# Kernel tuning notes

Hardware: AMD Instinct MI355X
Metric: run time of the kernel (lower is better)

The kernel has to match this reference:

```python
import jax, jax.numpy as jnp
import numpy as np

N_HEADS, N_LEVELS, N_POINTS, D_MODEL = 8, 3, 12, 64
PARAM_NAMES = ['vp0_w','vp0_b','vp1_w','vp1_b','so0_w','so0_b','so1_w','so1_b','so2_w','so2_b','so3_w','so3_b','aw0_w','aw0_b','aw1_w','aw1_b','aw2_w','aw2_b','aw3_w','aw3_b','op0_w','op0_b','op1_w','op1_b']

def _lrelu(x):
    return jnp.where(x >= 0, x, 0.1 * x)

def _conv(x, w, b):
    y = jax.lax.conv_general_dilated(x, w, (1, 1), 'SAME', dimension_numbers=('NCHW', 'OIHW', 'NCHW'))
    return y + b[None, :, None, None]

def _bilinear(img, px, py):
    # img [B,C,H,W]; px,py [B,Q] absolute pixel coords; zero padding (grid_sample 'zeros')
    B, C, H, W = img.shape
    flat = img.reshape(B, C, H * W)
    x0 = jnp.floor(px); y0 = jnp.floor(py)
    wx1 = px - x0; wy1 = py - y0
    def g(xi, yi, wgt):
        valid = (xi >= 0) & (xi <= W - 1) & (yi >= 0) & (yi <= H - 1)
        xi_c = jnp.clip(xi, 0, W - 1).astype(jnp.int32)
        yi_c = jnp.clip(yi, 0, H - 1).astype(jnp.int32)
        v = jnp.take_along_axis(flat, (yi_c * W + xi_c)[:, None, :], axis=2)
        return v * (wgt * valid)[:, None, :]
    return (g(x0, y0, (1 - wx1) * (1 - wy1)) + g(x0 + 1, y0, wx1 * (1 - wy1))
          + g(x0, y0 + 1, (1 - wx1) * wy1) + g(x0 + 1, y0 + 1, wx1 * wy1))

def _flow_warp(img, flow):
    # img [n,C,h,w]; flow [n,2,h,w] (x,y); matches grid_sample align_corners=True
    n, C, h, w = img.shape
    gy, gx = jnp.meshgrid(jnp.arange(h, dtype=img.dtype), jnp.arange(w, dtype=img.dtype), indexing='ij')
    px = (gx[None] + flow[:, 0]).reshape(n, h * w)
    py = (gy[None] + flow[:, 1]).reshape(n, h * w)
    return _bilinear(img, px, py).reshape(n, C, h, w)

def _forward(x, flow_1, flow_2, flip_flow_1, flip_flow_2, p):
    n, t, c, h, w = x.shape
    hw = h * w; THW = t * hw
    M, L, P, D = N_HEADS, N_LEVELS, N_POINTS, c // N_HEADS
    flow_cn1 = flow_1
    flow_cn2 = flow_1 + _flow_warp(flow_2, flow_1)
    flow_n1c, flow_n1n2 = flip_flow_1, flow_2
    flow_n2n1 = flip_flow_2
    flow_n2c = flip_flow_2 + _flow_warp(flip_flow_1, flip_flow_2)
    warp_cn1 = _flow_warp(x[:, 1], flow_cn1)
    warp_cn2 = _flow_warp(x[:, 2], flow_cn2)
    warp_n1c = _flow_warp(x[:, 0], flow_n1c)
    warp_n1n2 = _flow_warp(x[:, 2], flow_n1n2)
    warp_n2n1 = _flow_warp(x[:, 1], flow_n2n1)
    warp_n2c = _flow_warp(x[:, 0], flow_n2c)
    extra = jnp.concatenate([x[:, 0], warp_cn1, warp_cn2, warp_n1c, warp_n1n2, warp_n2n1, warp_n2c,
                             flow_cn1, flow_cn2, flow_n1c, flow_n1n2, flow_n2n1, flow_n2c], axis=1)
    value = _conv(_lrelu(_conv(x.reshape(n, t * c, h, w), p['vp0_w'], p['vp0_b'])), p['vp1_w'], p['vp1_b'])
    def head(e, pre):
        y = _lrelu(_conv(e, p[pre + '0_w'], p[pre + '0_b']))
        y = _lrelu(_conv(y, p[pre + '1_w'], p[pre + '1_b']))
        y = _lrelu(_conv(y, p[pre + '2_w'], p[pre + '2_b']))
        return _conv(y, p[pre + '3_w'], p[pre + '3_b'])
    so = head(extra, 'so')  # [n, L*M*L*P*2, h, w]
    aw = head(extra, 'aw')  # [n, L*M*L*P*9, h, w]
    so = so.reshape(n, t, -1, hw).transpose(0, 1, 3, 2).reshape(n, THW, M, L, P, 2)
    aw = aw.reshape(n, t, -1, hw).transpose(0, 1, 3, 2).reshape(n, THW, M, L * P * 9)
    aw = jax.nn.softmax(aw, axis=-1).reshape(n, THW, M, L, P * 9)
    # flow-guided offsets: add per-(query-frame, target-level) flow to learned offsets
    off = so.reshape(n, t, hw, M, L, P, 2)
    fz = jnp.zeros_like(flow_cn2)
    def lvl(f0, f1, f2):
        s = jnp.stack([f0, f1, f2], 1)  # [n,3,2,h,w]
        return s.transpose(0, 3, 4, 1, 2).reshape(n, hw, L, 2)[:, None, :, None, :, None, :]
    off = jnp.concatenate([
        off[:, 0:1] + lvl(fz, flow_cn1, flow_cn2),
        off[:, 1:2] + lvl(flow_n1c, fz, flow_n1n2),
        off[:, 2:3] + lvl(flow_n2c, flow_n2n1, fz)], axis=1).reshape(n, THW, M, L, P, 2)
    # 3x3 integer patch around each sampling point
    pi, pj = jnp.meshgrid(jnp.arange(-1, 2), jnp.arange(-1, 2), indexing='ij')
    patch = jnp.stack([pi, pj], -1).reshape(1, 1, 1, 1, 1, 9, 2).astype(off.dtype)
    off = (off[..., None, :] + patch).reshape(n, THW, M, L, P * 9, 2)
    # reference points (valid_ratios are all 1: full masks are zeros)
    ry, rx = jnp.meshgrid((jnp.arange(h) + 0.5) / h, (jnp.arange(w) + 0.5) / w, indexing='ij')
    ref = jnp.stack([rx, ry], -1).reshape(1, hw, 2).astype(off.dtype)
    ref = jnp.tile(ref, (1, t, 1))  # [1, THW, 2]
    norm = jnp.array([w, h], dtype=off.dtype)
    loc = ref[:, :, None, None, None, :] + off / norm  # [n,THW,M,L,P*9,2] normalized
    # multi-scale deformable attention (all L levels share (h,w)); align_corners=False, zeros pad
    P9 = P * 9
    v = value.reshape(n, t, c, hw).transpose(0, 1, 3, 2).reshape(n, THW, M, D)
    vl = v.reshape(n, L, hw, M, D).transpose(0, 3, 1, 4, 2).reshape(n * M * L, D, h, w)
    px = (loc[..., 0] * w - 0.5).transpose(0, 2, 3, 1, 4).reshape(n * M * L, THW * P9)
    py = (loc[..., 1] * h - 0.5).transpose(0, 2, 3, 1, 4).reshape(n * M * L, THW * P9)
    sampled = _bilinear(vl, px, py).reshape(n, M, L, D, THW, P9)
    out = jnp.einsum('nmldqp,nqmlp->nqmd', sampled, aw).reshape(n, THW, c)
    out = out.reshape(n, t, h, w, c).transpose(0, 1, 4, 2, 3).reshape(n, t * c, h, w)
    out = _conv(_lrelu(_conv(out, p['op0_w'], p['op0_b'])), p['op1_w'], p['op1_b'])
    return out.reshape(n, t, c, h, w) + x

def setup_inputs():
    key = jax.random.key(0)
    n, t, c, h, w = 1, 3, 64, 32, 32
    ks = jax.random.split(key, 24)
    d = {}
    d['x'] = jax.random.normal(ks[0], (n, t, c, h, w), jnp.float32)
    for i, name in enumerate(['flow_1', 'flow_2', 'flip_flow_1', 'flip_flow_2']):
        d[name] = jax.random.normal(ks[1 + i], (n, 2, h, w), jnp.float32)
    cin_extra = 7 * c + 12
    specs = [('vp0', t * c, t * c), ('vp1', t * c, t * c),
             ('so0', c, cin_extra), ('so1', c, c), ('so2', c, c), ('so3', N_LEVELS * N_HEADS * N_LEVELS * N_POINTS * 2, c),
             ('aw0', c, cin_extra), ('aw1', c, c), ('aw2', c, c), ('aw3', N_LEVELS * N_HEADS * N_LEVELS * N_POINTS * 9, c),
             ('op0', t * c, t * c), ('op1', t * c, t * c)]
    for i, (name, co, ci) in enumerate(specs):
        kw, kb = jax.random.split(ks[5 + i])
        std = (2.0 / (ci * 9)) ** 0.5
        d[name + '_w'] = jax.random.normal(kw, (co, ci, 3, 3), jnp.float32) * std
        d[name + '_b'] = jax.random.normal(kb, (co,), jnp.float32) * 0.01
    return d

def reference(x, flow_1, flow_2, flip_flow_1, flip_flow_2, vp0_w, vp0_b, vp1_w, vp1_b, so0_w, so0_b, so1_w, so1_b, so2_w, so2_b, so3_w, so3_b, aw0_w, aw0_b, aw1_w, aw1_b, aw2_w, aw2_b, aw3_w, aw3_b, op0_w, op0_b, op1_w, op1_b):
    p = dict(zip(PARAM_NAMES, (vp0_w, vp0_b, vp1_w, vp1_b, so0_w, so0_b, so1_w, so1_b, so2_w, so2_b, so3_w, so3_b, aw0_w, aw0_b, aw1_w, aw1_b, aw2_w, aw2_b, aw3_w, aw3_b, op0_w, op0_b, op1_w, op1_b)))
    return _forward(x, flow_1, flow_2, flip_flow_1, flip_flow_2, p)
```

## Files before the change

### kernel.cpp

```cpp
#include <hip/hip_runtime.h>
#include <math.h>

#define HW 1024

typedef __attribute__((ext_vector_type(8))) short bf16x8;
typedef __attribute__((ext_vector_type(4))) float floatx4;

__device__ __forceinline__ unsigned short f2bf(float f) {
    unsigned u = __float_as_uint(f);
    u += 0x7FFF + ((u >> 16) & 1);
    return (unsigned short)(u >> 16);
}
__device__ __forceinline__ float bf2f(unsigned short u) {
    return __uint_as_float(((unsigned)u) << 16);
}
__device__ __forceinline__ float bflo(unsigned u) { return __uint_as_float(u << 16); }
__device__ __forceinline__ float bfhi(unsigned u) { return __uint_as_float(u & 0xffff0000u); }

__device__ __forceinline__ float bilin32(const float* __restrict__ img, float px, float py) {
    float x0f = floorf(px), y0f = floorf(py);
    float wx = px - x0f, wy = py - y0f;
    bool vx0 = (x0f >= 0.f) && (x0f <= 31.f);
    bool vx1 = (x0f >= -1.f) && (x0f <= 30.f);
    bool vy0 = (y0f >= 0.f) && (y0f <= 31.f);
    bool vy1 = (y0f >= -1.f) && (y0f <= 30.f);
    int ix0 = (int)fminf(fmaxf(x0f, 0.f), 31.f);
    int iy0 = (int)fminf(fmaxf(y0f, 0.f), 31.f);
    int ix1 = (int)fminf(fmaxf(x0f + 1.f, 0.f), 31.f);
    int iy1 = (int)fminf(fmaxf(y0f + 1.f, 0.f), 31.f);
    float w00 = (1.f - wx) * (1.f - wy) * ((vx0 && vy0) ? 1.f : 0.f);
    float w01 = wx * (1.f - wy) * ((vx1 && vy0) ? 1.f : 0.f);
    float w10 = (1.f - wx) * wy * ((vx0 && vy1) ? 1.f : 0.f);
    float w11 = wx * wy * ((vx1 && vy1) ? 1.f : 0.f);
    return w00 * img[iy0 * 32 + ix0] + w01 * img[iy0 * 32 + ix1] +
           w10 * img[iy1 * 32 + ix0] + w11 * img[iy1 * 32 + ix1];
}

__device__ __forceinline__ float2 comp_flow(const float* __restrict__ fa,
                                            const float* __restrict__ fb, int pix) {
    int y = pix >> 5, x = pix & 31;
    float fx = fa[pix], fy = fa[HW + pix];
    float px = (float)x + fx, py = (float)y + fy;
    float2 r;
    r.x = fx + bilin32(fb, px, py);
    r.y = fy + bilin32(fb + HW, px, py);
    return r;
}

struct WD { const float* src; int cout, Cin, nCb, wbase, beg; };
struct PrepP {
    const float *x, *f1, *f2, *ff1, *ff2;
    float *fcn2, *fn2c;
    unsigned short *x_pad, *extra_pad, *wgt;
    WD wd[12];
};

__global__ __launch_bounds__(256) void prep_k(PrepP P) {
    __shared__ float wlds[16 * 288];
    const int b = blockIdx.x, tid = threadIdx.x;
    if (b < 192) {
        int idx = b * 256 + tid;
        int pix = idx / 48, c4 = idx - pix * 48;
        int y = pix >> 5, xx = pix & 31;
        int c0 = c4 * 4;
        ushort4 s;
        s.x = f2bf(P.x[(size_t)(c0 + 0) * HW + pix]);
        s.y = f2bf(P.x[(size_t)(c0 + 1) * HW + pix]);
        s.z = f2bf(P.x[(size_t)(c0 + 2) * HW + pix]);
        s.w = f2bf(P.x[(size_t)(c0 + 3) * HW + pix]);
        *(ushort4*)(&P.x_pad[(size_t)((y + 1) * 34 + xx + 1) * 192 + c0]) = s;
    } else if (b < 2112) {
        int idx = (b - 192) * 256 + tid;
        int ch = idx >> 10, pix = idx & 1023;
        int y = pix >> 5, xx = pix & 31;
        float v = 0.f;
        if (ch < 64) {
            v = P.x[(size_t)ch * HW + pix];
        } else if (ch < 448) {
            int grp = (ch - 64) >> 6;
            int c = (ch - 64) & 63;
            const float* src;
            float fx, fy;
            if (grp == 0)      { src = P.x + 64 * HW;  fx = P.f1[pix];  fy = P.f1[HW + pix]; }
            else if (grp == 1) { src = P.x + 128 * HW; float2 r = comp_flow(P.f1, P.f2, pix);  fx = r.x; fy = r.y; }
            else if (grp == 2) { src = P.x;            fx = P.ff1[pix]; fy = P.ff1[HW + pix]; }
            else if (grp == 3) { src = P.x + 128 * HW; fx = P.f2[pix];  fy = P.f2[HW + pix]; }
            else if (grp == 4) { src = P.x + 64 * HW;  fx = P.ff2[pix]; fy = P.ff2[HW + pix]; }
            else               { src = P.x;            float2 r = comp_flow(P.ff2, P.ff1, pix); fx = r.x; fy = r.y; }
            v = bilin32(src + c * HW, (float)xx + fx, (float)y + fy);
        } else if (ch < 460) {
            int fc = ch - 448;
            int which = fc >> 1, comp = fc & 1;
            if (which == 0)      v = P.f1[comp * HW + pix];
            else if (which == 1) { float2 r = comp_flow(P.f1, P.f2, pix);  v = comp ? r.y : r.x; }
            else if (which == 2) v = P.ff1[comp * HW + pix];
            else if (which == 3) v = P.f2[comp * HW + pix];
            else if (which == 4) v = P.ff2[comp * HW + pix];
            else                 { float2 r = comp_flow(P.ff2, P.ff1, pix); v = comp ? r.y : r.x; }
        }
        P.extra_pad[(size_t)((y + 1) * 34 + xx + 1) * 480 + ch] = f2bf(v);
    } else if (b < 2128) {
        int idx = (b - 2112) * 256 + tid;
        if (idx < 1024) {
            float2 r = comp_flow(P.f1, P.f2, idx);
            P.fcn2[idx] = r.x; P.fcn2[HW + idx] = r.y;
        } else if (idx < 2048) {
            int pix = idx - 1024;
            float2 r = comp_flow(P.ff2, P.ff1, pix);
            P.fn2c[pix] = r.x; P.fn2c[HW + pix] = r.y;
        }
    } else {
        int blk = b - 2128;
        int di = 0;
        while (di < 11 && blk >= P.wd[di + 1].beg) ++di;
        WD w = P.wd[di];
        int local = blk - w.beg;
        int co16 = local / w.nCb, cb = local - co16 * w.nCb;
        int cr0 = co16 * 16, ci0 = cb * 32;
        for (int i = tid; i < 16 * 288; i += 256) {
            int cr = i / 288, o = i - cr * 288;
            int crg = cr0 + cr, ci = ci0 + o / 9;
            float v = (crg < w.cout && ci < w.Cin)
                ? w.src[((size_t)crg * w.Cin + ci0) * 9 + o] : 0.f;
            wlds[i] = v;
        }
        __syncthreads();
        for (int e = tid; e < 9 * 512; e += 256) {
            int t = e >> 9, idx = e & 511;
            int j = idx & 7, lane = idx >> 3, q = lane >> 4, mm = lane & 15;
            P.wgt[((size_t)w.wbase + ((size_t)co16 * 9 + t) * w.nCb + cb) * 512 + idx] =
                f2bf(wlds[mm * 288 + (q * 8 + j) * 9 + t]);
        }
    }
}

struct CDesc {
    const unsigned short* in;
    const unsigned short* wgt;
    const float* bias;
    void* out;
    const float* residual;
    int Cpad, nCb, Cout, mode, cmod, relu, Mblocks;
};
struct CParam { CDesc d[4]; };

template<int PIXROWS>
__global__ __launch_bounds__(256) void conv_mfma_k(CParam P) {
    constexpr int TROWS = PIXROWS + 2;
    constexpr int TC = TROWS * 34 * 4;
    constexpr int ITRIPS = (TC + 255) / 256;
    constexpr int NTY = PIXROWS / 4;
    constexpr int NACC = NTY * 2;
    __shared__ unsigned short blds[TROWS * 34 * 40];
    __shared__ unsigned short wlds[36 * 512];

    int bx = blockIdx.x;
    int di = 0;
    while (bx >= P.d[di].Mblocks) { bx -= P.d[di].Mblocks; ++di; }
    const CDesc d = P.d[di];

    const int tid = threadIdx.x;
    const int w = tid >> 6, lane = tid & 63;
    const int lq = lane >> 4, ln = lane & 15;
    const int co0 = bx * 64;
    const int by = blockIdx.y, y0 = by * PIXROWS;
    const unsigned short* __restrict__ in = d.in;
    const unsigned short* __restrict__ wg = d.wgt;
    const int Cpad = d.Cpad, nCb = d.nCb;

    floatx4 acc[4][NACC];
#pragma unroll
    for (int mt = 0; mt < 4; ++mt)
#pragma unroll
        for (int nt = 0; nt < NACC; ++nt)
            acc[mt][nt] = (floatx4){0.f, 0.f, 0.f, 0.f};

    bf16x8 ireg[ITRIPS];
    bf16x8 wreg[9];

    auto load_regs = [&](int cb) {
        const int ci0 = cb << 5;
#pragma unroll
        for (int k = 0; k < ITRIPS; ++k) {
            int i = tid + k * 256;
            if (i < TC) {
                int r = i / 136, rem = i - r * 136, c = rem >> 2, g = rem & 3;
                ireg[k] = *(const bf16x8*)(in + (size_t)((y0 + r) * 34 + c) * Cpad + ci0 + g * 8);
            }
        }
#pragma unroll
        for (int k = 0; k < 9; ++k) {
            int i = tid + k * 256;
            int chunk = i >> 6, l16 = i & 63;
            int mt = chunk / 9, t = chunk - mt * 9;
            wreg[k] = *(const bf16x8*)(wg + ((size_t)(((co0 >> 4) + mt) * 9 + t) * nCb + cb) * 512 + l16 * 8);
        }
    };

    load_regs(0);

    for (int cb = 0; cb < nCb; ++cb) {
        __syncthreads();
#pragma unroll
        for (int k = 0; k < ITRIPS; ++k) {
            int i = tid + k * 256;
            if (i < TC) {
                int r = i / 136, rem = i - r * 136, c = rem >> 2, g = rem & 3;
                *(bf16x8*)(&blds[(r * 34 + c) * 40 + g * 8]) = ireg[k];
            }
        }
#pragma unroll
        for (int k = 0; k < 9; ++k) {
            int i = tid + k * 256;
            int chunk = i >> 6, l16 = i & 63;
            *(bf16x8*)(&wlds[chunk * 512 + l16 * 8]) = wreg[k];
        }
        __syncthreads();
        if (cb + 1 < nCb) load_regs(cb + 1);
        for (int t = 0; t < 9; ++t) {
            const int dy = t / 3, dx = t - dy * 3;
            bf16x8 bfr[NACC];
#pragma unroll
            for (int ty = 0; ty < NTY; ++ty)
#pragma unroll
                for (int tx = 0; tx < 2; ++tx) {
                    int yy = w * NTY + ty + dy;
                    int xx = tx * 16 + ln + dx;
                    bfr[ty * 2 + tx] = *(const bf16x8*)(&blds[(yy * 34 + xx) * 40 + lq * 8]);
                }
#pragma unroll
            for (int mt = 0; mt < 4; ++mt) {
                bf16x8 afr = *(const bf16x8*)(&wlds[(mt * 9 + t) * 512 + lane * 8]);
#pragma unroll
                for (int nt = 0; nt < NACC; ++nt)
                    acc[mt][nt] = __builtin_amdgcn_mfma_f32_16x16x32_bf16(afr, bfr[nt], acc[mt][nt], 0, 0, 0);
            }
        }
    }

#pragma unroll
    for (int mt = 0; mt < 4; ++mt) {
        const int co = co0 + mt * 16 + lq * 4;
        if (co >= d.Cout) continue;
        float bv[4];
#pragma unroll
        for (int r = 0; r < 4; ++r) bv[r] = d.bias[co + r];
#pragma unroll
        for (int nt = 0; nt < NACC; ++nt) {
            const int ty = nt >> 1, tx = nt & 1;
            const int pix = by * (PIXROWS * 32) + (w * NTY + ty) * 32 + tx * 16 + ln;
            float v[4];
#pragma unroll
            for (int r = 0; r < 4; ++r) {
                float vv = acc[mt][nt][r] + bv[r];
                if (d.relu) vv = (vv >= 0.f) ? vv : 0.1f * vv;
                v[r] = vv;
            }
            if (d.mode == 0) {
                float* o = (float*)d.out;
#pragma unroll
                for (int r = 0; r < 4; ++r) {
                    float vv = v[r];
                    if (d.residual) vv += d.residual[(size_t)(co + r) * HW + pix];
                    o[(size_t)(co + r) * HW + pix] = vv;
                }
            } else if (d.mode == 1) {
                int fq = co / d.cmod, cc = co - fq * d.cmod;
                *(float4*)((float*)d.out + ((size_t)fq * HW + pix) * d.cmod + cc) =
                    make_float4(v[0], v[1], v[2], v[3]);
            } else if (d.mode == 2) {
                int fq = co / d.cmod, cc = co - fq * d.cmod;
                ushort4 s4;
                s4.x = f2bf(v[0]); s4.y = f2bf(v[1]); s4.z = f2bf(v[2]); s4.w = f2bf(v[3]);
                *(ushort4*)((unsigned short*)d.out + ((size_t)fq * HW + pix) * d.cmod + cc) = s4;
            } else {
                int yy = (pix >> 5) + 1, xx = (pix & 31) + 1;
                ushort4 s4;
                s4.x = f2bf(v[0]); s4.y = f2bf(v[1]); s4.z = f2bf(v[2]); s4.w = f2bf(v[3]);
                *(ushort4*)((unsigned short*)d.out + (size_t)(yy * 34 + xx) * d.cmod + co) = s4;
            }
        }
    }
}

__global__ __launch_bounds__(256) void deform_attn_k(
    const unsigned short* __restrict__ value_b, const float* __restrict__ so_t,
    const unsigned short* __restrict__ aw_t,
    const float* __restrict__ flow_1, const float* __restrict__ flow_2,
    const float* __restrict__ flip_flow_1, const float* __restrict__ flip_flow_2,
    const float* __restrict__ flow_cn2, const float* __restrict__ flow_n2c,
    unsigned short* __restrict__ attn_pad)
{
    __shared__ unsigned short vlds[24576];
    __shared__ unsigned short pwlds[4][432];
    const int tid = threadIdx.x;
    const int wav = tid >> 6, lane = tid & 63;
    const int m = blockIdx.x & 7, qc = blockIdx.x >> 3;

    for (int i = tid; i < 3072; i += 256) {
        int l = i >> 10, p = i & 1023;
        *(bf16x8*)(&vlds[(size_t)i * 8]) =
            *(const bf16x8*)(value_b + ((size_t)((l * 8 + m) * 1024) + p) * 8);
    }
    __syncthreads();

    const int pp = lane & 15, gq = lane >> 4;
    const int gdy = (gq >> 1) * 2 - 1;
    const int gdx = (gq & 1) * 2 - 1;
    const bool selx = (gq & 1);
    const bool sely = (gq >> 1);

    for (int r = 0; r < 8; ++r) {
        const int q = qc * 32 + r * 4 + wav;
        const int f = q >> 10, pix = q & 1023;
        const int y = pix >> 5, x = pix & 31;

        float flx0 = 0.f, fly0 = 0.f, flx1 = 0.f, fly1 = 0.f, flx2 = 0.f, fly2 = 0.f;
        if (f == 0) {
            flx1 = flow_1[pix];      fly1 = flow_1[HW + pix];
            flx2 = flow_cn2[pix];    fly2 = flow_cn2[HW + pix];
        } else if (f == 1) {
            flx0 = flip_flow_1[pix]; fly0 = flip_flow_1[HW + pix];
            flx2 = flow_2[pix];      fly2 = flow_2[HW + pix];
        } else {
            flx0 = flow_n2c[pix];    fly0 = flow_n2c[HW + pix];
            flx1 = flip_flow_2[pix]; fly1 = flip_flow_2[HW + pix];
        }

        const unsigned short* awp = aw_t + (size_t)q * 2592 + m * 324;
        float av[6];
        float vmax = -1e30f;
#pragma unroll
        for (int it = 0; it < 6; ++it) {
            int j = lane + it * 64;
            float a = (j < 324) ? bf2f(awp[j]) : -1e30f;
            av[it] = a;
            vmax = fmaxf(vmax, a);
        }
#pragma unroll
        for (int off = 32; off; off >>= 1) vmax = fmaxf(vmax, __shfl_xor(vmax, off));
        float ssum = 0.f;
#pragma unroll
        for (int it = 0; it < 6; ++it) {
            int j = lane + it * 64;
            float e = (j < 324) ? __expf(av[it] - vmax) : 0.f;
            av[it] = e;
            ssum += e;
        }
#pragma unroll
        for (int off = 32; off; off >>= 1) ssum += __shfl_xor(ssum, off);
        const float inv = 1.f / ssum;

#pragma unroll
        for (int it = 0; it < 6; ++it) {
            int j = lane + it * 64;
            if (j < 324) {
                int pi = j / 9, k = j - pi * 9;
                pwlds[wav][pi * 12 + k] = f2bf(av[it] * inv);
            }
        }

        float acc[8];
#pragma unroll
        for (int dd = 0; dd < 8; ++dd) acc[dd] = 0.f;
        const float* sop = so_t + (size_t)q * 576 + m * 72;

#pragma unroll
        for (int pt = 0; pt < 3; ++pt) {
            int pi = pt * 16 + pp;
            if (pi < 36) {
                int l = pi / 12;
                float2 so2 = *(const float2*)(sop + pi * 2);
                float fx = (l == 0) ? flx0 : (l == 1) ? flx1 : flx2;
                float fy = (l == 0) ? fly0 : (l == 1) ? fly1 : fly2;
                float bxf = (float)x + so2.x + fx;
                float byf = (float)y + so2.y + fy;
                float x0f = floorf(bxf), y0f = floorf(byf);
                float wx = bxf - x0f, wy = byf - y0f;
                float ax = 1.f - wx, ay = 1.f - wy;
                int x0 = (int)fminf(fmaxf(x0f, -2.f), 34.f);
                int y0 = (int)fminf(fmaxf(y0f, -2.f), 34.f);

                const unsigned short* pr = &pwlds[wav][pi * 12];
                uint2 pv0 = *(const uint2*)(pr);
                uint2 pv1 = *(const uint2*)(pr + 4);
                float a0 = bflo(pv0.x), a1 = bfhi(pv0.x), a2 = bflo(pv0.y);
                float a3 = bfhi(pv0.y), a4 = bflo(pv1.x), a5 = bfhi(pv1.x);
                float a6 = bflo(pv1.y), a7 = bfhi(pv1.y), a8 = bf2f(pr[8]);

                float bs0a, bs0b, bs1a, bs1b, bs2a, bs2b;
                {
                    float b0, b1, b2, b3;
                    b0 = a0 * ax; b1 = a0 * wx + a3 * ax; b2 = a3 * wx + a6 * ax; b3 = a6 * wx;
                    bs0a = selx ? b2 : b0; bs0b = selx ? b3 : b1;
                    b0 = a1 * ax; b1 = a1 * wx + a4 * ax; b2 = a4 * wx + a7 * ax; b3 = a7 * wx;
                    bs1a = selx ? b2 : b0; bs1b = selx ? b3 : b1;
                    b0 = a2 * ax; b1 = a2 * wx + a5 * ax; b2 = a5 * wx + a8 * ax; b3 = a8 * wx;
                    bs2a = selx ? b2 : b0; bs2b = selx ? b3 : b1;
                }
                float c00, c01, c10, c11;
                {
                    float c0 = bs0a * ay, c1 = bs0a * wy + bs1a * ay;
                    float c2 = bs1a * wy + bs2a * ay, c3 = bs2a * wy;
                    c00 = sely ? c2 : c0; c10 = sely ? c3 : c1;
                    c0 = bs0b * ay; c1 = bs0b * wy + bs1b * ay;
                    c2 = bs1b * wy + bs2b * ay; c3 = bs2b * wy;
                    c01 = sely ? c2 : c0; c11 = sely ? c3 : c1;
                }
                float cg[2][2] = {{c00, c01}, {c10, c11}};
                const int vbase = l * 1024;
#pragma unroll
                for (int sy = 0; sy < 2; ++sy) {
#pragma unroll
                    for (int sx = 0; sx < 2; ++sx) {
                        int dy = gdy + sy, dx = gdx + sx;
                        float pyf = y0f + (float)dy, pxf = x0f + (float)dx;
                        bool v = (pxf >= 0.f) && (pxf <= 31.f) && (pyf >= 0.f) && (pyf <= 31.f);
                        int px = min(max(x0 + dx, 0), 31);
                        int py = min(max(y0 + dy, 0), 31);
                        float c = cg[sy][sx] * (v ? 1.f : 0.f);
                        uint4 vv = *(const uint4*)(&vlds[(size_t)(vbase + py * 32 + px) * 8]);
                        acc[0] = fmaf(c, bflo(vv.x), acc[0]);
                        acc[1] = fmaf(c, bfhi(vv.x), acc[1]);
                        acc[2] = fmaf(c, bflo(vv.y), acc[2]);
                        acc[3] = fmaf(c, bfhi(vv.y), acc[3]);
                        acc[4] = fmaf(c, bflo(vv.z), acc[4]);
                        acc[5] = fmaf(c, bfhi(vv.z), acc[5]);
                        acc[6] = fmaf(c, bflo(vv.w), acc[6]);
                        acc[7] = fmaf(c, bfhi(vv.w), acc[7]);
                    }
                }
            }
        }

#pragma unroll
        for (int dd = 0; dd < 8; ++dd) {
#pragma unroll
            for (int off = 32; off; off >>= 1) acc[dd] += __shfl_xor(acc[dd], off);
        }
        if (lane == 0) {
            unsigned short* op = attn_pad + (size_t)((y + 1) * 34 + x + 1) * 192 + f * 64 + m * 8;
            ushort4 s0, s1;
            s0.x = f2bf(acc[0]); s0.y = f2bf(acc[1]); s0.z = f2bf(acc[2]); s0.w = f2bf(acc[3]);
            s1.x = f2bf(acc[4]); s1.y = f2bf(acc[5]); s1.z = f2bf(acc[6]); s1.w = f2bf(acc[7]);
            *(ushort4*)(op) = s0;
            *(ushort4*)(op + 4) = s1;
        }
    }
}

extern "C" void kernel_launch(void* const* d_in, const int* in_sizes, int n_in,
                              void* d_out, int out_size, void* d_ws, size_t ws_size,
                              hipStream_t stream) {
    const float* x      = (const float*)d_in[0];
    const float* flow_1 = (const float*)d_in[1];
    const float* flow_2 = (const float*)d_in[2];
    const float* flip_1 = (const float*)d_in[3];
    const float* flip_2 = (const float*)d_in[4];
    const float* vp0_w = (const float*)d_in[5];  const float* vp0_b = (const float*)d_in[6];
    const float* vp1_w = (const float*)d_in[7];  const float* vp1_b = (const float*)d_in[8];
    const float* so0_w = (const float*)d_in[9];  const float* so0_b = (const float*)d_in[10];
    const float* so1_w = (const float*)d_in[11]; const float* so1_b = (const float*)d_in[12];
    const float* so2_w = (const float*)d_in[13]; const float* so2_b = (const float*)d_in[14];
    const float* so3_w = (const float*)d_in[15]; const float* so3_b = (const float*)d_in[16];
    const float* aw0_w = (const float*)d_in[17]; const float* aw0_b = (const float*)d_in[18];
    const float* aw1_w = (const float*)d_in[19]; const float* aw1_b = (const float*)d_in[20];
    const float* aw2_w = (const float*)d_in[21]; const float* aw2_b = (const float*)d_in[22];
    const float* aw3_w = (const float*)d_in[23]; const float* aw3_b = (const float*)d_in[24];
    const float* op0_w = (const float*)d_in[25]; const float* op0_b = (const float*)d_in[26];
    const float* op1_w = (const float*)d_in[27]; const float* op1_b = (const float*)d_in[28];
    float* out = (float*)d_out;
    (void)ws_size; (void)in_sizes; (void)n_in; (void)out_size;

    float* fws = (float*)d_ws;
    float* flow_cn2 = fws;
    float* flow_n2c = flow_cn2 + 2048;
    unsigned short* value_b = (unsigned short*)(flow_n2c + 2048);
    float* so_t     = (float*)(value_b + 196608);
    unsigned short* uws = (unsigned short*)(so_t + 1769472);
    unsigned short* x_pad     = uws;
    unsigned short* vp0h      = x_pad + 1156 * 192;
    unsigned short* extra_pad = vp0h + 1156 * 192;
    unsigned short* s1 = extra_pad + 1156 * 480;
    unsigned short* a1 = s1 + 1156 * 64;
    unsigned short* s2 = a1 + 1156 * 64;
    unsigned short* a2 = s2 + 1156 * 64;
    unsigned short* attn_pad = a2 + 1156 * 64;
    unsigned short* op0h     = attn_pad + 1156 * 192;
    const size_t pad_shorts = (size_t)1156 * (192 * 4 + 480 + 64 * 4);
    unsigned short* aw_t = op0h + 1156 * 192;
    unsigned short* wgt  = aw_t + (size_t)3072 * 2592;

    hipMemsetAsync(x_pad, 0, pad_shorts * sizeof(unsigned short), stream);

    PrepP pp;
    pp.x = x; pp.f1 = flow_1; pp.f2 = flow_2; pp.ff1 = flip_1; pp.ff2 = flip_2;
    pp.fcn2 = flow_cn2; pp.fn2c = flow_n2c;
    pp.x_pad = x_pad; pp.extra_pad = extra_pad; pp.wgt = wgt;
    pp.wd[0]  = {vp0_w, 192, 192, 6,     0,    0};
    pp.wd[1]  = {vp1_w, 192, 192, 6,   648,   72};
    pp.wd[2]  = {so0_w,  64, 460, 15, 1296,  144};
    pp.wd[3]  = {aw0_w,  64, 460, 15, 1836,  204};
    pp.wd[4]  = {so1_w,  64,  64, 2,  2376,  264};
    pp.wd[5]  = {aw1_w,  64,  64, 2,  2448,  272};
    pp.wd[6]  = {so2_w,  64,  64, 2,  2520,  280};
    pp.wd[7]  = {aw2_w,  64,  64, 2,  2592,  288};
    pp.wd[8]  = {so3_w, 1728, 64, 2,  2664,  296};
    pp.wd[9]  = {aw3_w, 7776, 64, 2,  4608,  512};
    pp.wd[10] = {op0_w, 192, 192, 6, 13392, 1488};
    pp.wd[11] = {op1_w, 192, 192, 6, 14040, 1560};
    prep_k<<<3760, 256, 0, stream>>>(pp);

    const int BIG = 1 << 30;
    CDesc nul = {nullptr, nullptr, nullptr, nullptr, nullptr, 0, 0, 0, 0, 0, 0, BIG};

    {
        CParam cp;
        cp.d[0] = {x_pad,     wgt + (size_t)0 * 512,    vp0_b, vp0h, nullptr, 192, 6,  192, 3, 192, 1, 3};
        cp.d[1] = {extra_pad, wgt + (size_t)1296 * 512, so0_b, s1,   nullptr, 480, 15, 64,  3, 64,  1, 1};
        cp.d[2] = {extra_pad, wgt + (size_t)1836 * 512, aw0_b, a1,   nullptr, 480, 15, 64,  3, 64,  1, 1};
        cp.d[3] = nul;
        conv_mfma_k<4><<<dim3(5, 8), 256, 0, stream>>>(cp);
    }
    {
        CParam cp;
        cp.d[0] = {vp0h, wgt + (size_t)648 * 512,  vp1_b, value_b, nullptr, 192, 6, 192, 2, 8,  0, 3};
        cp.d[1] = {s1,   wgt + (size_t)2376 * 512, so1_b, s2,      nullptr, 64,  2, 64,  3, 64, 1, 1};
        cp.d[2] = {a1,   wgt + (size_t)2448 * 512, aw1_b, a2,      nullptr, 64,  2, 64,  3, 64, 1, 1};
        cp.d[3] = nul;
        conv_mfma_k<4><<<dim3(5, 8), 256, 0, stream>>>(cp);
    }
    {
        CParam cp;
        cp.d[0] = {s2, wgt + (size_t)2520 * 512, so2_b, s1, nullptr, 64, 2, 64, 3, 64, 1, 1};
        cp.d[1] = {a2, wgt + (size_t)2592 * 512, aw2_b, a1, nullptr, 64, 2, 64, 3, 64, 1, 1};
        cp.d[2] = nul; cp.d[3] = nul;
        conv_mfma_k<4><<<dim3(2, 8), 256, 0, stream>>>(cp);
    }
    {
        CParam cp;
        cp.d[0] = {s1, wgt + (size_t)2664 * 512, so3_b, so_t, nullptr, 64, 2, 1728, 1, 576,  0, 27};
        cp.d[1] = {a1, wgt + (size_t)4608 * 512, aw3_b, aw_t, nullptr, 64, 2, 7776, 2, 2592, 0, 122};
        cp.d[2] = nul; cp.d[3] = nul;
        conv_mfma_k<8><<<dim3(149, 4), 256, 0, stream>>>(cp);
    }

    deform_attn_k<<<768, 256, 0, stream>>>(value_b, so_t, aw_t,
                                           flow_1, flow_2, flip_1, flip_2,
                                           flow_cn2, flow_n2c, attn_pad);

    {
        CParam cp;
        cp.d[0] = {attn_pad, wgt + (size_t)13392 * 512, op0_b, op0h, nullptr, 192, 6, 192, 3, 192, 1, 3};
        cp.d[1] = nul; cp.d[2] = nul; cp.d[3] = nul;
        conv_mfma_k<4><<<dim3(3, 8), 256, 0, stream>>>(cp);
    }
    {
        CParam cp;
        cp.d[0] = {op0h, wgt + (size_t)14040 * 512, op1_b, out, x, 192, 6, 192, 0, 0, 0, 3};
        cp.d[1] = nul; cp.d[2] = nul; cp.d[3] = nul;
        conv_mfma_k<4><<<dim3(3, 8), 256, 0, stream>>>(cp);
    }
}
```

Before: 291.9 us.

## Narrow conv output-channel tile to raise block count and zero only pad borders

The conv kernel gains a COBLK template parameter. The small convs now use 16 output channels per block instead of 64, so they launch four times as many blocks, which raises occupancy on a mostly idle GPU. The full-buffer hipMemsetAsync of the padded activation buffers is replaced by 16 extra prep blocks that zero only the 1-pixel halo border of each buffer. In exchange, input tiles are reloaded more often per output channel and weight reuse per block drops.

Result: faster. 269.9 us (-7.5%).

```diff
diff --git a/kernel.cpp b/kernel.cpp
--- a/kernel.cpp
+++ b/kernel.cpp
@@ -109,8 +109,23 @@
             float2 r = comp_flow(P.ff2, P.ff1, pix);
             P.fn2c[pix] = r.x; P.fn2c[HW + pix] = r.y;
         }
+    } else if (b < 2144) {
+        const int chans[9] = {192, 192, 480, 64, 64, 64, 64, 192, 192};
+        size_t offs[9]; size_t a = 0;
+        for (int i = 0; i < 9; ++i) { offs[i] = a; a += (size_t)1156 * chans[i]; }
+        int bb = b - 2128;
+        for (int item = bb; item < 9 * 132; item += 16) {
+            int buf = item / 132, i = item - buf * 132;
+            int py, px;
+            if (i < 34) { py = 0; px = i; }
+            else if (i < 68) { py = 33; px = i - 34; }
+            else { int j = i - 68; py = 1 + (j >> 1); px = (j & 1) ? 33 : 0; }
+            int C = chans[buf];
+            unsigned short* p = P.x_pad + offs[buf] + (size_t)(py * 34 + px) * C;
+            for (int c = tid; c < C; c += 256) p[c] = 0;
+        }
     } else {
-        int blk = b - 2128;
+        int blk = b - 2144;
         int di = 0;
         while (di < 11 && blk >= P.wd[di + 1].beg) ++di;
         WD w = P.wd[di];
@@ -144,15 +159,18 @@
 };
 struct CParam { CDesc d[4]; };
 
-template<int PIXROWS>
+template<int PIXROWS, int COBLK>
 __global__ __launch_bounds__(256) void conv_mfma_k(CParam P) {
     constexpr int TROWS = PIXROWS + 2;
     constexpr int TC = TROWS * 34 * 4;
     constexpr int ITRIPS = (TC + 255) / 256;
     constexpr int NTY = PIXROWS / 4;
     constexpr int NACC = NTY * 2;
+    constexpr int MT = COBLK / 16;
+    constexpr int WN = MT * 9 * 64;
+    constexpr int WTRIPS = (WN + 255) / 256;
     __shared__ unsigned short blds[TROWS * 34 * 40];
-    __shared__ unsigned short wlds[36 * 512];
+    __shared__ unsigned short wlds[MT * 9 * 512];
 
     int bx = blockIdx.x;
     int di = 0;
@@ -162,21 +180,21 @@
     const int tid = threadIdx.x;
     const int w = tid >> 6, lane = tid & 63;
     const int lq = lane >> 4, ln = lane & 15;
-    const int co0 = bx * 64;
+    const int co0 = bx * COBLK;
     const int by = blockIdx.y, y0 = by * PIXROWS;
     const unsigned short* __restrict__ in = d.in;
     const unsigned short* __restrict__ wg = d.wgt;
     const int Cpad = d.Cpad, nCb = d.nCb;
 
-    floatx4 acc[4][NACC];
-#pragma unroll
-    for (int mt = 0; mt < 4; ++mt)
+    floatx4 acc[MT][NACC];
+#pragma unroll
+    for (int mt = 0; mt < MT; ++mt)
 #pragma unroll
         for (int nt = 0; nt < NACC; ++nt)
             acc[mt][nt] = (floatx4){0.f, 0.f, 0.f, 0.f};
 
     bf16x8 ireg[ITRIPS];
-    bf16x8 wreg[9];
+    bf16x8 wreg[WTRIPS];
 
     auto load_regs = [&](int cb) {
         const int ci0 = cb << 5;
@@ -189,11 +207,13 @@
             }
         }
 #pragma unroll
-        for (int k = 0; k < 9; ++k) {
+        for (int k = 0; k < WTRIPS; ++k) {
             int i = tid + k * 256;
-            int chunk = i >> 6, l16 = i & 63;
-            int mt = chunk / 9, t = chunk - mt * 9;
-            wreg[k] = *(const bf16x8*)(wg + ((size_t)(((co0 >> 4) + mt) * 9 + t) * nCb + cb) * 512 + l16 * 8);
+            if (i < WN) {
+                int chunk = i >> 6, l16 = i & 63;
+                int mt = chunk / 9, t = chunk - mt * 9;
+                wreg[k] = *(const bf16x8*)(wg + ((size_t)(((co0 >> 4) + mt) * 9 + t) * nCb + cb) * 512 + l16 * 8);
+            }
         }
     };
 
@@ -210,10 +230,12 @@
             }
         }
 #pragma unroll
-        for (int k = 0; k < 9; ++k) {
+        for (int k = 0; k < WTRIPS; ++k) {
             int i = tid + k * 256;
-            int chunk = i >> 6, l16 = i & 63;
-            *(bf16x8*)(&wlds[chunk * 512 + l16 * 8]) = wreg[k];
+            if (i < WN) {
+                int chunk = i >> 6, l16 = i & 63;
+                *(bf16x8*)(&wlds[chunk * 512 + l16 * 8]) = wreg[k];
+            }
         }
         __syncthreads();
         if (cb + 1 < nCb) load_regs(cb + 1);
@@ -229,7 +251,7 @@
                     bfr[ty * 2 + tx] = *(const bf16x8*)(&blds[(yy * 34 + xx) * 40 + lq * 8]);
                 }
 #pragma unroll
-            for (int mt = 0; mt < 4; ++mt) {
+            for (int mt = 0; mt < MT; ++mt) {
                 bf16x8 afr = *(const bf16x8*)(&wlds[(mt * 9 + t) * 512 + lane * 8]);
 #pragma unroll
                 for (int nt = 0; nt < NACC; ++nt)
@@ -239,7 +261,7 @@
     }
 
 #pragma unroll
-    for (int mt = 0; mt < 4; ++mt) {
+    for (int mt = 0; mt < MT; ++mt) {
         const int co = co0 + mt * 16 + lq * 4;
         if (co >= d.Cout) continue;
         float bv[4];
@@ -487,11 +509,8 @@
     unsigned short* a2 = s2 + 1156 * 64;
     unsigned short* attn_pad = a2 + 1156 * 64;
     unsigned short* op0h     = attn_pad + 1156 * 192;
-    const size_t pad_shorts = (size_t)1156 * (192 * 4 + 480 + 64 * 4);
     unsigned short* aw_t = op0h + 1156 * 192;
     unsigned short* wgt  = aw_t + (size_t)3072 * 2592;
-
-    hipMemsetAsync(x_pad, 0, pad_shorts * sizeof(unsigned short), stream);
 
     PrepP pp;
     pp.x = x; pp.f1 = flow_1; pp.f2 = flow_2; pp.ff1 = flip_1; pp.ff2 = flip_2;
@@ -509,40 +528,40 @@
     pp.wd[9]  = {aw3_w, 7776, 64, 2,  4608,  512};
     pp.wd[10] = {op0_w, 192, 192, 6, 13392, 1488};
     pp.wd[11] = {op1_w, 192, 192, 6, 14040, 1560};
-    prep_k<<<3760, 256, 0, stream>>>(pp);
+    prep_k<<<3776, 256, 0, stream>>>(pp);
 
     const int BIG = 1 << 30;
     CDesc nul = {nullptr, nullptr, nullptr, nullptr, nullptr, 0, 0, 0, 0, 0, 0, BIG};
 
     {
         CParam cp;
-        cp.d[0] = {x_pad,     wgt + (size_t)0 * 512,    vp0_b, vp0h, nullptr, 192, 6,  192, 3, 192, 1, 3};
-        cp.d[1] = {extra_pad, wgt + (size_t)1296 * 512, so0_b, s1,   nullptr, 480, 15, 64,  3, 64,  1, 1};
-        cp.d[2] = {extra_pad, wgt + (size_t)1836 * 512, aw0_b, a1,   nullptr, 480, 15, 64,  3, 64,  1, 1};
+        cp.d[0] = {x_pad,     wgt + (size_t)0 * 512,    vp0_b, vp0h, nullptr, 192, 6,  192, 3, 192, 1, 12};
+        cp.d[1] = {extra_pad, wgt + (size_t)1296 * 512, so0_b, s1,   nullptr, 480, 15, 64,  3, 64,  1, 4};
+        cp.d[2] = {extra_pad, wgt + (size_t)1836 * 512, aw0_b, a1,   nullptr, 480, 15, 64,  3, 64,  1, 4};
         cp.d[3] = nul;
-        conv_mfma_k<4><<<dim3(5, 8), 256, 0, stream>>>(cp);
+        conv_mfma_k<4, 16><<<dim3(20, 8), 256, 0, stream>>>(cp);
     }
     {
         CParam cp;
-        cp.d[0] = {vp0h, wgt + (size_t)648 * 512,  vp1_b, value_b, nullptr, 192, 6, 192, 2, 8,  0, 3};
-        cp.d[1] = {s1,   wgt + (size_t)2376 * 512, so1_b, s2,      nullptr, 64,  2, 64,  3, 64, 1, 1};
-        cp.d[2] = {a1,   wgt + (size_t)2448 * 512, aw1_b, a2,      nullptr, 64,  2, 64,  3, 64, 1, 1};
+        cp.d[0] = {vp0h, wgt + (size_t)648 * 512,  vp1_b, value_b, nullptr, 192, 6, 192, 2, 8,  0, 12};
+        cp.d[1] = {s1,   wgt + (size_t)2376 * 512, so1_b, s2,      nullptr, 64,  2, 64,  3, 64, 1, 4};
+        cp.d[2] = {a1,   wgt + (size_t)2448 * 512, aw1_b, a2,      nullptr, 64,  2, 64,  3, 64, 1, 4};
         cp.d[3] = nul;
-        conv_mfma_k<4><<<dim3(5, 8), 256, 0, stream>>>(cp);
+        conv_mfma_k<4, 16><<<dim3(20, 8), 256, 0, stream>>>(cp);
     }
     {
         CParam cp;
-        cp.d[0] = {s2, wgt + (size_t)2520 * 512, so2_b, s1, nullptr, 64, 2, 64, 3, 64, 1, 1};
-        cp.d[1] = {a2, wgt + (size_t)2592 * 512, aw2_b, a1, nullptr, 64, 2, 64, 3, 64, 1, 1};
+        cp.d[0] = {s2, wgt + (size_t)2520 * 512, so2_b, s1, nullptr, 64, 2, 64, 3, 64, 1, 4};
+        cp.d[1] = {a2, wgt + (size_t)2592 * 512, aw2_b, a1, nullptr, 64, 2, 64, 3, 64, 1, 4};
         cp.d[2] = nul; cp.d[3] = nul;
-        conv_mfma_k<4><<<dim3(2, 8), 256, 0, stream>>>(cp);
+        conv_mfma_k<4, 16><<<dim3(8, 8), 256, 0, stream>>>(cp);
     }
     {
         CParam cp;
         cp.d[0] = {s1, wgt + (size_t)2664 * 512, so3_b, so_t, nullptr, 64, 2, 1728, 1, 576,  0, 27};
         cp.d[1] = {a1, wgt + (size_t)4608 * 512, aw3_b, aw_t, nullptr, 64, 2, 7776, 2, 2592, 0, 122};
         cp.d[2] = nul; cp.d[3] = nul;
-        conv_mfma_k<8><<<dim3(149, 4), 256, 0, stream>>>(cp);
+        conv_mfma_k<8, 64><<<dim3(149, 4), 256, 0, stream>>>(cp);
     }
 
     deform_attn_k<<<768, 256, 0, stream>>>(value_b, so_t, aw_t,
@@ -551,14 +570,14 @@
 
     {
         CParam cp;
-        cp.d[0] = {attn_pad, wgt + (size_t)13392 * 512, op0_b, op0h, nullptr, 192, 6, 192, 3, 192, 1, 3};
+        cp.d[0] = {attn_pad, wgt + (size_t)13392 * 512, op0_b, op0h, nullptr, 192, 6, 192, 3, 192, 1, 12};
         cp.d[1] = nul; cp.d[2] = nul; cp.d[3] = nul;
-        conv_mfma_k<4><<<dim3(3, 8), 256, 0, stream>>>(cp);
+        conv_mfma_k<4, 16><<<dim3(12, 8), 256, 0, stream>>>(cp);
     }
     {
         CParam cp;
-        cp.d[0] = {op0h, wgt + (size_t)14040 * 512, op1_b, out, x, 192, 6, 192, 0, 0, 0, 3};
+        cp.d[0] = {op0h, wgt + (size_t)14040 * 512, op1_b, out, x, 192, 6, 192, 0, 0, 0, 12};
         cp.d[1] = nul; cp.d[2] = nul; cp.d[3] = nul;
-        conv_mfma_k<4><<<dim3(3, 8), 256, 0, stream>>>(cp);
-    }
-}
+        conv_mfma_k<4, 16><<<dim3(12, 8), 256, 0, stream>>>(cp);
+    }
+}
```
